# Kernel tuning notes

Hardware: AMD Instinct MI355X
Metric: run time of the kernel (lower is better)

Reference implementation:

```python
import jax, jax.numpy as jnp
import numpy as np

MC_SAMPLES = 32  # k neighbors
BIG = 1e8


def _swish(x):
    return x * jax.nn.sigmoid(x)


def setup_inputs() -> dict:
    key = jax.random.key(0)
    ks = jax.random.split(key, 8)
    bs, n, d, c = 8, 1024, 3, 64
    cmco_ci, hid = 16, 32
    abq_pairs = jax.random.normal(ks[0], (bs, n, n, d), dtype=jnp.float32)
    vals = jax.random.normal(ks[1], (bs, n, c), dtype=jnp.float32)
    mask = jnp.ones((bs, n), dtype=bool)
    s = 0.1
    return {
        "abq_pairs": abq_pairs,
        "vals": vals,
        "mask": mask,
        "W1": jax.random.normal(ks[2], (d, hid), dtype=jnp.float32) * s,
        "b1": jnp.zeros((hid,), jnp.float32),
        "W2": jax.random.normal(ks[3], (hid, hid), dtype=jnp.float32) * s,
        "b2": jnp.zeros((hid,), jnp.float32),
        "W3": jax.random.normal(ks[4], (hid, cmco_ci), dtype=jnp.float32) * s,
        "b3": jnp.zeros((cmco_ci,), jnp.float32),
        "Wl": jax.random.normal(ks[5], (c * cmco_ci, c), dtype=jnp.float32) * s,
        "bl": jnp.zeros((c,), jnp.float32),
    }


def reference(abq_pairs, vals, mask, W1, b1, W2, b2, W3, b3, Wl, bl):
    bs, n, _, d = abq_pairs.shape
    c = vals.shape[-1]
    k = min(MC_SAMPLES, n)

    # --- extract_neighborhood (knn branch, ds_frac=1 so queries = all points) ---
    # Trivial group distance = norm over last dim of abq pairs: (bs,n,n)
    dists = jnp.linalg.norm(abq_pairs, axis=-1)
    dists = jnp.where(mask[:, None, :], dists, BIG)
    _, nbhd_idx = jax.lax.top_k(-dists, k)  # smallest-k -> (bs, n, k)

    # gather neighbor pairwise embeddings: (bs, n, k, d)
    nbhd_abq = jnp.take_along_axis(abq_pairs, nbhd_idx[..., None], axis=2)
    # gather neighbor values and mask per batch: (bs, n, k, c), (bs, n, k)
    nbhd_vals = jax.vmap(lambda v, i: v[i])(vals, nbhd_idx)
    nbhd_mask = jax.vmap(lambda m, i: m[i])(mask, nbhd_idx) & mask[:, :, None]

    h = _swish(nbhd_abq @ W1 + b1)
    h = _swish(h @ W2 + b2)
    penult_kernel_weights = _swish(h @ W3 + b3)  # (bs, n, k, 16)

    # --- masked weighted aggregation (generalized PointConv trick) ---
    mW = jnp.where(nbhd_mask[..., None], penult_kernel_weights, 0.0)
    mV = jnp.where(nbhd_mask[..., None], nbhd_vals, 0.0)
    # vals^T @ weights -> (bs, n, c, 16) -> (bs, n, c*16)
    partial = jnp.einsum("bmkc,bmkp->bmcp", mV, mW).reshape(bs, n, -1)
    convolved = partial @ Wl + bl  # (bs, n, c)

    # zero out invalid query points
    return jnp.where(mask[..., None], convolved, 0.0)
```

## Files before the change

### kernel.cpp

```cpp
#include <hip/hip_runtime.h>
#include <math.h>


#define NPTS 1024
#define KNB  32
#define CCH  64
#define HID  32
#define PCH  16

#define OFF_PACK    196608
#define OFF_NB      4456448
#define PACKN       1808
#define OFF_WLB_U16 262144

typedef __bf16        bf16x8 __attribute__((ext_vector_type(8)));
typedef float         f32x4  __attribute__((ext_vector_type(4)));
typedef unsigned int  uint4v __attribute__((ext_vector_type(4)));

__device__ __forceinline__ float swishf(float x) {
    return x * __builtin_amdgcn_rcpf(1.0f + __expf(-x));
}

__device__ __forceinline__ unsigned bf16rne(float f) {
    unsigned u = __float_as_uint(f);
    return (u + 0x7fffu + ((u >> 16) & 1u)) >> 16;
}

__global__ __launch_bounds__(256) void lieconv_pack(
    const float* __restrict__ W1, const float* __restrict__ b1,
    const float* __restrict__ W2, const float* __restrict__ b2,
    const float* __restrict__ W3, const float* __restrict__ b3,
    const float* __restrict__ Wl, float* __restrict__ ws)
{
    const int tid = threadIdx.x;
    if (blockIdx.x == 0) {
        float* pack = ws + OFF_PACK;
        for (int idx = tid; idx < PACKN; idx += 256) {
            float v;
            if (idx < 128) {
                int i4 = idx >> 4, rem = idx & 15, r = rem >> 2, u = rem & 3;
                v = (r < 3) ? W1[r * 32 + i4 * 4 + u] : b1[i4 * 4 + u];
            } else if (idx < 1792) {
                int oi = idx - 128;
                int o = oi / 52, t = oi - o * 52;
                if (t < 32)       v = W2[t * 32 + o];
                else if (t < 48)  v = W3[o * 16 + (t - 32)];
                else if (t == 48) v = b2[o];
                else              v = 0.0f;
            } else {
                v = b3[idx - 1792];
            }
            pack[idx] = v;
        }
    } else {
        const int t   = (blockIdx.x - 1) * 256 + tid;
        const int g   = t >> 6, l = t & 63;
        const int k0  = (g >> 2) * 32 + ((l >> 4) << 3);
        const int col = ((g & 3) << 4) + (l & 15);
        unsigned us[8];
#pragma unroll
        for (int j = 0; j < 8; ++j)
            us[j] = bf16rne(Wl[(size_t)(k0 + j) * 64 + col]);
        uint4 pk;
        pk.x = us[0] | (us[1] << 16);
        pk.y = us[2] | (us[3] << 16);
        pk.z = us[4] | (us[5] << 16);
        pk.w = us[6] | (us[7] << 16);
        *(uint4*)((unsigned short*)ws + OFF_WLB_U16 + (size_t)t * 8) = pk;
    }
}

__global__ __launch_bounds__(256, 8) void lieconv_knn(
    const float* __restrict__ abq, unsigned short* __restrict__ sel_out,
    float* __restrict__ nbbuf)
{
    __shared__ int s_cand[4][64];
    const int tid  = threadIdx.x;
    const int lane = tid & 63;
    const int w    = tid >> 6;
    const int row  = blockIdx.x * 4 + w;
    const float* __restrict__ rowp = abq + (size_t)row * (NPTS * 3);

    float kf[16];
#pragma unroll
    for (int q = 0; q < 16; ++q) {
        int j = q * 64 + lane;
        float x = rowp[j * 3 + 0];
        float y = rowp[j * 3 + 1];
        float z = rowp[j * 3 + 2];
        kf[q] = fmaf(x, x, fmaf(y, y, z * z));
    }
    float kmax = kf[0];
#pragma unroll
    for (int q = 1; q < 16; ++q) kmax = fmaxf(kmax, kf[q]);
#pragma unroll
    for (int off = 32; off > 0; off >>= 1)
        kmax = fmaxf(kmax, __shfl_xor(kmax, off, 64));

    float lo = 0.0f, hi = kmax * 1.000001f + 1e-30f, T = hi;
    for (int it = 0; it < 28; ++it) {
        float mid = 0.5f * (lo + hi);
        int c = 0;
#pragma unroll
        for (int q = 0; q < 16; ++q)
            c += __popcll(__ballot(kf[q] < mid));
        if (c < KNB)      lo = mid;
        else if (c > 40)  hi = mid;
        else { T = mid; break; }
        T = hi;
    }
    float Tcut = T * 1.000001f;

    const unsigned long long lmask = (1ull << lane) - 1ull;
    int base = 0;
#pragma unroll
    for (int q = 0; q < 16; ++q) {
        bool p = kf[q] < Tcut;
        unsigned long long mk = __ballot(p);
        int pos = base + __popcll(mk & lmask);
        if (p && pos < 64) s_cand[w][pos] = q * 64 + lane;
        base += __popcll(mk);
    }
    int ncand = (base < 64) ? base : 64;

    unsigned long long ci = ~0ull;
    int ji = 0x7fffffff;
    if (lane < ncand) {
        ji = s_cand[w][lane];
        double x = (double)rowp[ji * 3 + 0];
        double y = (double)rowp[ji * 3 + 1];
        double z = (double)rowp[ji * 3 + 2];
        double ki = (x * x + y * y) + z * z;
        ci = ((unsigned long long)__double_as_longlong(ki) & ~1023ull) | (unsigned)ji;
    }
    int rank = 0;
#pragma unroll
    for (int t = 0; t < 64; ++t) {
        unsigned long long ct = __shfl(ci, t, 64);
        rank += (ct < ci) ? 1 : 0;
    }
    bool sel = (lane < ncand) && (rank < KNB);
    unsigned long long mk = __ballot(sel);
    if (sel) {
        int pos = (int)((size_t)row * KNB) + __popcll(mk & lmask);
        sel_out[pos] = (unsigned short)ji;
        float* nb = nbbuf + (size_t)pos * 3;
        nb[0] = rowp[ji * 3 + 0];
        nb[1] = rowp[ji * 3 + 1];
        nb[2] = rowp[ji * 3 + 2];
    }
}

#define WVS 20

__global__ __launch_bounds__(256, 4) void lieconv_tail(
    const float* __restrict__ vals, const unsigned short* __restrict__ sel,
    const float* __restrict__ ws_ro, const float* __restrict__ Wl,
    const float* __restrict__ bl, float* __restrict__ out)
{
    __shared__ __align__(16) float s_mem[4096 + 256 * WVS];
    float* s_pack = s_mem;
    float* s_wv   = s_mem + 4096;
    char*  spb    = (char*)s_mem;

    const int tid  = threadIdx.x;
    const int lane = tid & 63;
    const int w    = tid >> 6;
    const size_t r0 = (size_t)blockIdx.x * 8;

#pragma unroll
    for (int u = 0; u < 8; ++u) {
        int idx = u * 256 + tid;
        if (idx < PACKN) s_pack[idx] = ws_ro[OFF_PACK + idx];
    }
    __syncthreads();

    {
        const size_t P = (size_t)blockIdx.x * 256 + tid;
        const float* __restrict__ nb = ws_ro + OFF_NB + P * 3;
        float x = nb[0], y = nb[1], z = nb[2];

        const float4* __restrict__ w1p = (const float4*)s_pack;
        const float4* __restrict__ opk = (const float4*)s_pack + 32;
        const float4* __restrict__ b3q = (const float4*)(s_pack + 1792);

        float h1[32];
#pragma unroll
        for (int i4 = 0; i4 < 8; ++i4) {
            float4 qa = w1p[i4 * 4 + 0];
            float4 qb = w1p[i4 * 4 + 1];
            float4 qc = w1p[i4 * 4 + 2];
            float4 qd = w1p[i4 * 4 + 3];
            h1[i4 * 4 + 0] = swishf(fmaf(x, qa.x, fmaf(y, qb.x, fmaf(z, qc.x, qd.x))));
            h1[i4 * 4 + 1] = swishf(fmaf(x, qa.y, fmaf(y, qb.y, fmaf(z, qc.y, qd.y))));
            h1[i4 * 4 + 2] = swishf(fmaf(x, qa.z, fmaf(y, qb.z, fmaf(z, qc.z, qd.z))));
            h1[i4 * 4 + 3] = swishf(fmaf(x, qa.w, fmaf(y, qb.w, fmaf(z, qc.w, qd.w))));
        }

        float wv[16];
        {
            float4 q0 = b3q[0], q1 = b3q[1], q2 = b3q[2], q3 = b3q[3];
            wv[0]=q0.x; wv[1]=q0.y; wv[2]=q0.z; wv[3]=q0.w;
            wv[4]=q1.x; wv[5]=q1.y; wv[6]=q1.z; wv[7]=q1.w;
            wv[8]=q2.x; wv[9]=q2.y; wv[10]=q2.z; wv[11]=q2.w;
            wv[12]=q3.x; wv[13]=q3.y; wv[14]=q3.z; wv[15]=q3.w;
        }
#pragma unroll
        for (int o = 0; o < 32; ++o) {
            const float4* q = opk + o * 13;
            float acc = q[12].x;
#pragma unroll
            for (int n = 0; n < 8; ++n) {
                float4 qq = q[n];
                acc = fmaf(h1[n * 4 + 0], qq.x, acc);
                acc = fmaf(h1[n * 4 + 1], qq.y, acc);
                acc = fmaf(h1[n * 4 + 2], qq.z, acc);
                acc = fmaf(h1[n * 4 + 3], qq.w, acc);
            }
            float h2 = swishf(acc);
#pragma unroll
            for (int n = 0; n < 4; ++n) {
                float4 qq = q[8 + n];
                wv[n * 4 + 0] = fmaf(h2, qq.x, wv[n * 4 + 0]);
                wv[n * 4 + 1] = fmaf(h2, qq.y, wv[n * 4 + 1]);
                wv[n * 4 + 2] = fmaf(h2, qq.z, wv[n * 4 + 2]);
                wv[n * 4 + 3] = fmaf(h2, qq.w, wv[n * 4 + 3]);
            }
        }
        float* wo = &s_wv[tid * WVS];
#pragma unroll
        for (int n = 0; n < 4; ++n)
            *(float4*)&wo[n * 4] = make_float4(swishf(wv[n * 4 + 0]), swishf(wv[n * 4 + 1]),
                                               swishf(wv[n * 4 + 2]), swishf(wv[n * 4 + 3]));
    }
    __syncthreads();

    const int p4    = (lane & 3) * 4;
    const int cbase = lane >> 2;
#pragma unroll
    for (int rr = 0; rr < 2; ++rr) {
        const int lr = w * 2 + rr;
        const size_t R = r0 + lr;
        const float* __restrict__ valsb = vals + (R >> 10) * (size_t)(NPTS * CCH);
        const unsigned short* __restrict__ selr = sel + R * KNB;

        int jj_l = (int)selr[lane & 31];

        float acc[4][4];
#pragma unroll
        for (int it = 0; it < 4; ++it)
#pragma unroll
            for (int e = 0; e < 4; ++e) acc[it][e] = 0.0f;

#pragma unroll 8
        for (int kk = 0; kk < KNB; ++kk) {
            int jj = __shfl(jj_l, kk, 64);
            float4 wq = *(const float4*)&s_wv[(lr * 32 + kk) * WVS + p4];
            const float* vr = valsb + (size_t)jj * CCH + cbase;
#pragma unroll
            for (int it = 0; it < 4; ++it) {
                float v = vr[16 * it];
                acc[it][0] = fmaf(v, wq.x, acc[it][0]);
                acc[it][1] = fmaf(v, wq.y, acc[it][1]);
                acc[it][2] = fmaf(v, wq.z, acc[it][2]);
                acc[it][3] = fmaf(v, wq.w, acc[it][3]);
            }
        }
        const unsigned xr = (unsigned)((lr & 7) << 4);
#pragma unroll
        for (int it = 0; it < 4; ++it) {
            int c = cbase + 16 * it;
            unsigned kb  = (unsigned)(c * 32 + p4 * 2);
            unsigned off = (unsigned)(lr * 2048) + (kb ^ xr);
            uint2 pkv;
            pkv.x = bf16rne(acc[it][0]) | (bf16rne(acc[it][1]) << 16);
            pkv.y = bf16rne(acc[it][2]) | (bf16rne(acc[it][3]) << 16);
            *(uint2*)(spb + off) = pkv;
        }
    }
    __syncthreads();

    {
        const int arow = lane & 15;
        const int kgrp = lane >> 4;
        const bf16x8* __restrict__ wlb8 =
            (const bf16x8*)((const unsigned short*)ws_ro + OFF_WLB_U16) + (w * 64 + lane);

        uint4v zz = {0u, 0u, 0u, 0u};
        const bf16x8 a0 = __builtin_bit_cast(bf16x8, zz);
        f32x4 acc = {0.0f, 0.0f, 0.0f, 0.0f};

        const unsigned x     = (unsigned)((arow & 7) << 4);
        const unsigned abase = (unsigned)(arow * 2048) + ((unsigned)(kgrp * 16) ^ (x & 48u));
        const unsigned xl    = x & 64u;
#pragma unroll 8
        for (int s = 0; s < 32; ++s) {
            bf16x8 a = a0;
            if (arow < 8)
                a = *(const bf16x8*)(spb + (abase + (((unsigned)(s * 64)) ^ xl)));
            bf16x8 b = wlb8[(size_t)s * 256];
            acc = __builtin_amdgcn_mfma_f32_16x16x32_bf16(a, b, acc, 0, 0, 0);
        }
        if (kgrp < 2) {
            const int cc   = w * 16 + arow;
            const float bias = bl[cc];
#pragma unroll
            for (int r4 = 0; r4 < 4; ++r4)
                out[(r0 + kgrp * 4 + r4) * 64 + cc] = acc[r4] + bias;
        }
    }
}

extern "C" void kernel_launch(void* const* d_in, const int* in_sizes, int n_in,
                              void* d_out, int out_size, void* d_ws, size_t ws_size,
                              hipStream_t stream)
{
    const float* abq  = (const float*)d_in[0];
    const float* vals = (const float*)d_in[1];
    const float* W1 = (const float*)d_in[3];
    const float* b1 = (const float*)d_in[4];
    const float* W2 = (const float*)d_in[5];
    const float* b2 = (const float*)d_in[6];
    const float* W3 = (const float*)d_in[7];
    const float* b3 = (const float*)d_in[8];
    const float* Wl = (const float*)d_in[9];
    const float* bl = (const float*)d_in[10];
    float* out = (float*)d_out;

    float* ws = (float*)d_ws;
    unsigned short* sel = (unsigned short*)d_ws;
    float* nbbuf = ws + OFF_NB;

    hipLaunchKernelGGL(lieconv_pack, dim3(33), dim3(256), 0, stream,
                       W1, b1, W2, b2, W3, b3, Wl, ws);
    hipLaunchKernelGGL(lieconv_knn, dim3(2048), dim3(256), 0, stream,
                       abq, sel, nbbuf);
    hipLaunchKernelGGL(lieconv_tail, dim3(1024), dim3(256), 0, stream,
                       vals, sel, ws, Wl, bl, out);
}
```

Before: 223.0 us.

## Fuse kNN selection into tail kernel, keeping neighbor indices in shared memory

Merges the kNN selection kernel into the weight-net and aggregation kernel. Each wave now handles two query rows, and the selected indices and neighbor coordinates stay in LDS instead of making a round trip through a global workspace. This removes one launch and the global writes and reads of the selection buffers. In exchange, each block handles 8 rows instead of 16 waves each doing one row, so kNN parallelism per block drops, and occupancy is tied to the tail kernel's launch bounds and larger LDS footprint.

New measurement: 208.3 us. 1.07x faster.

```diff
diff --git a/kernel.cpp b/kernel.cpp
--- a/kernel.cpp
+++ b/kernel.cpp
@@ -9,7 +9,6 @@
 #define PCH  16
 
 #define OFF_PACK    196608
-#define OFF_NB      4456448
 #define PACKN       1808
 #define OFF_WLB_U16 262144
 
@@ -70,98 +69,19 @@
     }
 }
 
-__global__ __launch_bounds__(256, 8) void lieconv_knn(
-    const float* __restrict__ abq, unsigned short* __restrict__ sel_out,
-    float* __restrict__ nbbuf)
+#define WVS 20
+
+__global__ __launch_bounds__(256, 4) void lieconv_fused(
+    const float* __restrict__ abq, const float* __restrict__ vals,
+    const float* __restrict__ ws_ro, const float* __restrict__ bl,
+    float* __restrict__ out)
 {
-    __shared__ int s_cand[4][64];
-    const int tid  = threadIdx.x;
-    const int lane = tid & 63;
-    const int w    = tid >> 6;
-    const int row  = blockIdx.x * 4 + w;
-    const float* __restrict__ rowp = abq + (size_t)row * (NPTS * 3);
-
-    float kf[16];
-#pragma unroll
-    for (int q = 0; q < 16; ++q) {
-        int j = q * 64 + lane;
-        float x = rowp[j * 3 + 0];
-        float y = rowp[j * 3 + 1];
-        float z = rowp[j * 3 + 2];
-        kf[q] = fmaf(x, x, fmaf(y, y, z * z));
-    }
-    float kmax = kf[0];
-#pragma unroll
-    for (int q = 1; q < 16; ++q) kmax = fmaxf(kmax, kf[q]);
-#pragma unroll
-    for (int off = 32; off > 0; off >>= 1)
-        kmax = fmaxf(kmax, __shfl_xor(kmax, off, 64));
-
-    float lo = 0.0f, hi = kmax * 1.000001f + 1e-30f, T = hi;
-    for (int it = 0; it < 28; ++it) {
-        float mid = 0.5f * (lo + hi);
-        int c = 0;
-#pragma unroll
-        for (int q = 0; q < 16; ++q)
-            c += __popcll(__ballot(kf[q] < mid));
-        if (c < KNB)      lo = mid;
-        else if (c > 40)  hi = mid;
-        else { T = mid; break; }
-        T = hi;
-    }
-    float Tcut = T * 1.000001f;
-
-    const unsigned long long lmask = (1ull << lane) - 1ull;
-    int base = 0;
-#pragma unroll
-    for (int q = 0; q < 16; ++q) {
-        bool p = kf[q] < Tcut;
-        unsigned long long mk = __ballot(p);
-        int pos = base + __popcll(mk & lmask);
-        if (p && pos < 64) s_cand[w][pos] = q * 64 + lane;
-        base += __popcll(mk);
-    }
-    int ncand = (base < 64) ? base : 64;
-
-    unsigned long long ci = ~0ull;
-    int ji = 0x7fffffff;
-    if (lane < ncand) {
-        ji = s_cand[w][lane];
-        double x = (double)rowp[ji * 3 + 0];
-        double y = (double)rowp[ji * 3 + 1];
-        double z = (double)rowp[ji * 3 + 2];
-        double ki = (x * x + y * y) + z * z;
-        ci = ((unsigned long long)__double_as_longlong(ki) & ~1023ull) | (unsigned)ji;
-    }
-    int rank = 0;
-#pragma unroll
-    for (int t = 0; t < 64; ++t) {
-        unsigned long long ct = __shfl(ci, t, 64);
-        rank += (ct < ci) ? 1 : 0;
-    }
-    bool sel = (lane < ncand) && (rank < KNB);
-    unsigned long long mk = __ballot(sel);
-    if (sel) {
-        int pos = (int)((size_t)row * KNB) + __popcll(mk & lmask);
-        sel_out[pos] = (unsigned short)ji;
-        float* nb = nbbuf + (size_t)pos * 3;
-        nb[0] = rowp[ji * 3 + 0];
-        nb[1] = rowp[ji * 3 + 1];
-        nb[2] = rowp[ji * 3 + 2];
-    }
-}
-
-#define WVS 20
-
-__global__ __launch_bounds__(256, 4) void lieconv_tail(
-    const float* __restrict__ vals, const unsigned short* __restrict__ sel,
-    const float* __restrict__ ws_ro, const float* __restrict__ Wl,
-    const float* __restrict__ bl, float* __restrict__ out)
-{
-    __shared__ __align__(16) float s_mem[4096 + 256 * WVS];
+    __shared__ __align__(16) float s_mem[10112];
     float* s_pack = s_mem;
     float* s_wv   = s_mem + 4096;
     char*  spb    = (char*)s_mem;
+    float* s_nb   = s_mem + 9216;
+    unsigned short* s_sel = (unsigned short*)(s_mem + 9984);
 
     const int tid  = threadIdx.x;
     const int lane = tid & 63;
@@ -173,12 +93,90 @@
         int idx = u * 256 + tid;
         if (idx < PACKN) s_pack[idx] = ws_ro[OFF_PACK + idx];
     }
+
+    {
+        int* s_cand = (int*)(s_mem + 4096) + w * 64;
+        const unsigned long long lmask = (1ull << lane) - 1ull;
+        for (int rr = 0; rr < 2; ++rr) {
+            const int lr = w * 2 + rr;
+            const float* __restrict__ rowp = abq + (r0 + lr) * (size_t)(NPTS * 3);
+
+            float kf[16];
+#pragma unroll
+            for (int q = 0; q < 16; ++q) {
+                int j = q * 64 + lane;
+                float x = rowp[j * 3 + 0];
+                float y = rowp[j * 3 + 1];
+                float z = rowp[j * 3 + 2];
+                kf[q] = fmaf(x, x, fmaf(y, y, z * z));
+            }
+            float kmax = kf[0];
+#pragma unroll
+            for (int q = 1; q < 16; ++q) kmax = fmaxf(kmax, kf[q]);
+#pragma unroll
+            for (int off = 32; off > 0; off >>= 1)
+                kmax = fmaxf(kmax, __shfl_xor(kmax, off, 64));
+
+            float lo = 0.0f, hi = kmax * 1.000001f + 1e-30f, T = hi;
+            for (int it = 0; it < 28; ++it) {
+                float mid = 0.5f * (lo + hi);
+                int c = 0;
+#pragma unroll
+                for (int q = 0; q < 16; ++q)
+                    c += __popcll(__ballot(kf[q] < mid));
+                if (c < KNB)      lo = mid;
+                else if (c > 40)  hi = mid;
+                else { T = mid; break; }
+                T = hi;
+            }
+            float Tcut = T * 1.000001f;
+
+            int base = 0;
+#pragma unroll
+            for (int q = 0; q < 16; ++q) {
+                bool p = kf[q] < Tcut;
+                unsigned long long mk = __ballot(p);
+                int pos = base + __popcll(mk & lmask);
+                if (p && pos < 64) s_cand[pos] = q * 64 + lane;
+                base += __popcll(mk);
+            }
+            int ncand = (base < 64) ? base : 64;
+
+            unsigned long long ci = ~0ull;
+            int ji = 0x7fffffff;
+            double xd = 0.0, yd = 0.0, zd = 0.0;
+            if (lane < ncand) {
+                ji = s_cand[lane];
+                xd = (double)rowp[ji * 3 + 0];
+                yd = (double)rowp[ji * 3 + 1];
+                zd = (double)rowp[ji * 3 + 2];
+                double ki = (xd * xd + yd * yd) + zd * zd;
+                ci = ((unsigned long long)__double_as_longlong(ki) & ~1023ull) | (unsigned)ji;
+            }
+            int rank = 0;
+#pragma unroll
+            for (int t = 0; t < 64; ++t) {
+                unsigned long long ct = __shfl(ci, t, 64);
+                rank += (ct < ci) ? 1 : 0;
+            }
+            bool selb = (lane < ncand) && (rank < KNB);
+            unsigned long long mk = __ballot(selb);
+            if (selb) {
+                int pos = lr * KNB + __popcll(mk & lmask);
+                s_sel[pos] = (unsigned short)ji;
+                float* nbp = s_nb + pos * 3;
+                nbp[0] = (float)xd;
+                nbp[1] = (float)yd;
+                nbp[2] = (float)zd;
+            }
+        }
+    }
     __syncthreads();
 
     {
-        const size_t P = (size_t)blockIdx.x * 256 + tid;
-        const float* __restrict__ nb = ws_ro + OFF_NB + P * 3;
-        float x = nb[0], y = nb[1], z = nb[2];
+        float x = s_nb[tid * 3 + 0];
+        float y = s_nb[tid * 3 + 1];
+        float z = s_nb[tid * 3 + 2];
 
         const float4* __restrict__ w1p = (const float4*)s_pack;
         const float4* __restrict__ opk = (const float4*)s_pack + 32;
@@ -242,9 +240,8 @@
         const int lr = w * 2 + rr;
         const size_t R = r0 + lr;
         const float* __restrict__ valsb = vals + (R >> 10) * (size_t)(NPTS * CCH);
-        const unsigned short* __restrict__ selr = sel + R * KNB;
-
-        int jj_l = (int)selr[lane & 31];
+
+        int jj_l = (int)s_sel[lr * 32 + (lane & 31)];
 
         float acc[4][4];
 #pragma unroll
@@ -328,13 +325,9 @@
     float* out = (float*)d_out;
 
     float* ws = (float*)d_ws;
-    unsigned short* sel = (unsigned short*)d_ws;
-    float* nbbuf = ws + OFF_NB;
 
     hipLaunchKernelGGL(lieconv_pack, dim3(33), dim3(256), 0, stream,
                        W1, b1, W2, b2, W3, b3, Wl, ws);
-    hipLaunchKernelGGL(lieconv_knn, dim3(2048), dim3(256), 0, stream,
-                       abq, sel, nbbuf);
-    hipLaunchKernelGGL(lieconv_tail, dim3(1024), dim3(256), 0, stream,
-                       vals, sel, ws, Wl, bl, out);
-}
+    hipLaunchKernelGGL(lieconv_fused, dim3(1024), dim3(256), 0, stream,
+                       abq, vals, ws, bl, out);
+}
```
